# Kernel optimization log

Hardware: AMD Instinct MI355X
Metric: run time of the kernel (lower is better)

Reference implementation:

```python
import jax, jax.numpy as jnp
import numpy as np

B, T, C = 2, 4096, 768
H = 12
D = C // H  # head_dim = 64
SCALE = np.sqrt(D).astype(np.float32)


def setup_inputs() -> dict:
    key = jax.random.key(0)
    ks = jax.random.split(key, 5)
    s = 0.02
    return {
        "x": jax.random.normal(ks[0], (B, T, C), dtype=jnp.float32),
        "Wqkv": jax.random.normal(ks[1], (C, 3 * C), dtype=jnp.float32) * s,
        "bqkv": jnp.zeros((3 * C,), dtype=jnp.float32),
        "Wout": jax.random.normal(ks[2], (C, C), dtype=jnp.float32) * s,
        "bout": jnp.zeros((C,), dtype=jnp.float32),
    }


def reference(x, Wqkv, bqkv, Wout, bout):
    Bx, Tx, Cx = x.shape
    qkv = x @ Wqkv + bqkv                                   # [B,T,3C]
    qkv = qkv.reshape(Bx, Tx, 3, H, D)
    q, k, v = [jnp.moveaxis(qkv[:, :, i], 2, 1) for i in range(3)]  # each [B,H,T,D]
    attn = jnp.einsum("bhqd,bhkd->bhqk", q, k) / SCALE      # [B,H,T,T]
    causal = jnp.tril(jnp.ones((Tx, Tx), dtype=bool))
    attn = jnp.where(causal, attn, jnp.float32(-jnp.inf))
    attn = jax.nn.softmax(attn, axis=-1)
    out = jnp.einsum("bhqk,bhkd->bhqd", attn, v)            # [B,H,T,D]
    out = jnp.moveaxis(out, 1, 2).reshape(Bx, Tx, Cx)       # [B,T,C]
    return out @ Wout + bout
```

## Files before the change

kernel.cpp:

```cpp
#include <hip/hip_runtime.h>
#include <hip/hip_bf16.h>

#define T_DIM 4096
#define H_N 12
#define D_H 64
#define C_DIM 768
#define B_N 2

typedef short bf16x8 __attribute__((ext_vector_type(8)));
typedef float f32x4 __attribute__((ext_vector_type(4)));

__device__ __forceinline__ short f2bf(float f) {
    union { float f; unsigned u; } x; x.f = f;
    unsigned r = x.u + 0x7fffu + ((x.u >> 16) & 1u);
    return (short)(r >> 16);
}
__device__ __forceinline__ unsigned pk2bf(float a, float b) {
    union { float f; unsigned u; } x, y; x.f = a; y.f = b;
    unsigned ua = x.u + 0x7fffu + ((x.u >> 16) & 1u);
    unsigned ub = y.u + 0x7fffu + ((y.u >> 16) & 1u);
    return (ua >> 16) | (ub & 0xffff0000u);
}
__device__ __forceinline__ unsigned pktrunc(float lo, float hi) {
    union { float f; unsigned u; } a, b; a.f = lo; b.f = hi;
    return __builtin_amdgcn_perm(b.u, a.u, 0x07060302u);
}
__device__ __forceinline__ float bf2f(short s) {
    union { unsigned u; float f; } x; x.u = ((unsigned)(unsigned short)s) << 16;
    return x.f;
}

__device__ __forceinline__ void async_copy16(const void* g, void* l) {
    __builtin_amdgcn_global_load_lds(
        (const __attribute__((address_space(1))) unsigned*)g,
        (__attribute__((address_space(3))) unsigned*)l, 16, 0, 0);
}

#define Q_SCALE 0.18033688011112042f

__global__ __launch_bounds__(256) void xconv_kernel(
    const float* __restrict__ x, short* __restrict__ xb)
{
    size_t i = ((size_t)blockIdx.x * 256 + threadIdx.x) * 8;
    float4 a = *(const float4*)(x + i);
    float4 b = *(const float4*)(x + i + 4);
    unsigned pk[4];
    pk[0] = pk2bf(a.x, a.y); pk[1] = pk2bf(a.z, a.w);
    pk[2] = pk2bf(b.x, b.y); pk[3] = pk2bf(b.z, b.w);
    *(uint4*)(xb + i) = *(uint4*)pk;
}

__global__ __launch_bounds__(256) void wtrans_kernel(
    const float* __restrict__ W, short* __restrict__ Wt, int K, int N)
{
    const int wave = threadIdx.x >> 6, lane = threadIdx.x & 63;
    const int n = blockIdx.x * 256 + wave * 64 + lane;
    const int k0 = blockIdx.y * 128;
    for (int k = k0; k < k0 + 128; k += 8) {
        unsigned pk[4];
#pragma unroll
        for (int j = 0; j < 4; ++j)
            pk[j] = pk2bf(W[(size_t)(k + 2 * j) * N + n],
                          W[(size_t)(k + 2 * j + 1) * N + n]);
        *(uint4*)(Wt + (size_t)n * K + k) = *(uint4*)pk;
    }
}

__global__ __launch_bounds__(256) void qkv_kernel(
    const short* __restrict__ xb, const short* __restrict__ Wb,
    const float* __restrict__ bias,
    short* __restrict__ Qo, short* __restrict__ Ko, short* __restrict__ Vto)
{
    __shared__ short As[128 * 32];
    __shared__ short Bs[128 * 32];
    __shared__ short Vs[64][136];

    const int tid  = threadIdx.x;
    const int wave = tid >> 6, lane = tid & 63;
    const int quad = lane >> 4, l16 = lane & 15;
    const int wm = wave >> 1, wn = wave & 1;
    const int m0 = blockIdx.y * 128, n0 = blockIdx.x * 128;
    const int lrow = lane >> 2, lcc = lane & 3;

    f32x4 acc[4][4];
#pragma unroll
    for (int i = 0; i < 4; ++i)
#pragma unroll
        for (int j = 0; j < 4; ++j) acc[i][j] = (f32x4){0.f, 0.f, 0.f, 0.f};

    for (int k0 = 0; k0 < 768; k0 += 32) {
        __syncthreads();
#pragma unroll
        for (int i = 0; i < 2; ++i) {
            const int sbase = wave * 128 + i * 64;
            const int row = wave * 32 + i * 16 + lrow;
            async_copy16(xb + (size_t)(m0 + row) * 768 + k0 + lcc * 8, &As[sbase * 8]);
            async_copy16(Wb + (size_t)(n0 + row) * 768 + k0 + lcc * 8, &Bs[sbase * 8]);
        }
        asm volatile("s_waitcnt vmcnt(0)" ::: "memory");
        __syncthreads();

        bf16x8 af[4], bfr[4];
#pragma unroll
        for (int t = 0; t < 4; ++t)
            af[t] = *(const bf16x8*)&As[(wm * 64 + t * 16 + l16) * 32 + quad * 8];
#pragma unroll
        for (int t = 0; t < 4; ++t)
            bfr[t] = *(const bf16x8*)&Bs[(wn * 64 + t * 16 + l16) * 32 + quad * 8];
#pragma unroll
        for (int mt = 0; mt < 4; ++mt)
#pragma unroll
            for (int nt = 0; nt < 4; ++nt)
                acc[mt][nt] = __builtin_amdgcn_mfma_f32_16x16x32_bf16(
                    af[mt], bfr[nt], acc[mt][nt], 0, 0, 0);
    }

    if (n0 < 1536) {
#pragma unroll
        for (int nt = 0; nt < 4; ++nt) {
            int n = n0 + wn * 64 + nt * 16 + l16;
            float bv = bias[n];
            int which = n >= 768;
            int cw = n - which * 768;
            int h = cw >> 6, d = cw & 63;
            float scale = which ? 1.0f : Q_SCALE;
            short* dst = which ? Ko : Qo;
#pragma unroll
            for (int mt = 0; mt < 4; ++mt) {
#pragma unroll
                for (int reg = 0; reg < 4; ++reg) {
                    int m = m0 + wm * 64 + mt * 16 + quad * 4 + reg;
                    int b = m >> 12, t = m & 4095;
                    dst[(size_t)((b * H_N + h) * T_DIM + t) * D_H + d] =
                        f2bf((acc[mt][nt][reg] + bv) * scale);
                }
            }
        }
    } else {
        const int b = m0 >> 12, t0 = m0 & 4095;
        for (int p = 0; p < 2; ++p) {
            if (wn == p) {
#pragma unroll
                for (int nt = 0; nt < 4; ++nt) {
                    int n = n0 + wn * 64 + nt * 16 + l16;
                    float bv = bias[n];
#pragma unroll
                    for (int mt = 0; mt < 4; ++mt)
#pragma unroll
                        for (int reg = 0; reg < 4; ++reg)
                            Vs[nt * 16 + l16][wm * 64 + mt * 16 + quad * 4 + reg] =
                                f2bf(acc[mt][nt][reg] + bv);
                }
            }
            __syncthreads();
            int hh = ((n0 - 1536) >> 6) + p;
#pragma unroll
            for (int cc = tid; cc < 512; cc += 256) {
                int d = cc >> 3, part = cc & 7;
                bf16x8 v0 = *(const bf16x8*)&Vs[d][part * 16];
                bf16x8 v1 = *(const bf16x8*)&Vs[d][part * 16 + 8];
                size_t dst = ((size_t)(b * H_N + hh) * D_H + d) * T_DIM + t0 + part * 16;
                *(bf16x8*)(Vto + dst) = v0;
                *(bf16x8*)(Vto + dst + 8) = v1;
            }
            __syncthreads();
        }
    }
}

__global__ __launch_bounds__(256) void attn_partial_kernel(
    const short* __restrict__ Q, const short* __restrict__ K,
    const short* __restrict__ Vt, short* __restrict__ Opart,
    float* __restrict__ Lbuf)
{
    __shared__ short KsT[2][4096];
    __shared__ short VsT[2][4096];
    __shared__ short Ps[4][32][76];

    const int tid  = threadIdx.x;
    const int wave = tid >> 6, lane = tid & 63;
    const int quad = lane >> 4, l16 = lane & 15;
    const int bh = blockIdx.y;
    const int rr = blockIdx.x;

    int qj, ci;
    if (rr < 12) { qj = 12 + rr; ci = 0; }
    else if (rr < 28) { int t = rr - 12; qj = 24 + (t >> 1); ci = t & 1; }
    else {
        int t = rr - 28;
        if (t < 8) { int g = t >> 1, b = t & 1; int m = 12 - g;
                     qj = b ? (11 + m) : (m - 1); }
        else { int tt = t - 8; int g = tt / 3, b = tt - 3 * g; int m = 8 - g;
               qj = (b == 0) ? (m - 1) : ((b == 1) ? (11 + m) : (23 + m)); }
        ci = qj / 12;
    }
    const int q0 = qj * 128;
    const int kvStart = ci * 1536;
    const int kvEnd = min(kvStart + 1536, q0 + 128);
    const int ntiles = (kvEnd - kvStart) >> 6;
    const int off = (qj < 12) ? qj : ((qj < 24) ? 12 + (qj - 12) * 2
                                               : 36 + (qj - 24) * 3);
    const int s = bh * 60 + off + ci;
    const size_t base = (size_t)bh * T_DIM * D_H;
    const int row0 = q0 + wave * 32;

    bf16x8 qf[2][2];
#pragma unroll
    for (int qt = 0; qt < 2; ++qt)
#pragma unroll
        for (int ks = 0; ks < 2; ++ks)
            qf[qt][ks] = *(const bf16x8*)(
                Q + base + (size_t)(row0 + qt * 16 + l16) * 64 + ks * 32 + quad * 8);

    bf16x8 ones;
#pragma unroll
    for (int j = 0; j < 8; ++j) ones[j] = (short)0x3F80;

    f32x4 oacc[2][4], lacc[2];
#pragma unroll
    for (int qt = 0; qt < 2; ++qt) {
        lacc[qt] = (f32x4){0.f, 0.f, 0.f, 0.f};
#pragma unroll
        for (int nt = 0; nt < 4; ++nt) oacc[qt][nt] = (f32x4){0.f, 0.f, 0.f, 0.f};
    }

    const int srow = (wave * 128 + lane) >> 3;
    const int scol0 = (lane & 7) ^ (srow & 7);
    const int srow1 = (wave * 128 + 64 + lane) >> 3;
    const int scol1 = (lane & 7) ^ (srow1 & 7);

    {
        const int kv0 = kvStart;
        async_copy16(K + base + (size_t)(kv0 + srow) * 64 + scol0 * 8,
                     &KsT[0][(wave * 128) * 8]);
        async_copy16(Vt + base + (size_t)srow * T_DIM + kv0 + scol0 * 8,
                     &VsT[0][(wave * 128) * 8]);
        async_copy16(K + base + (size_t)(kv0 + srow1) * 64 + scol1 * 8,
                     &KsT[0][(wave * 128 + 64) * 8]);
        async_copy16(Vt + base + (size_t)srow1 * T_DIM + kv0 + scol1 * 8,
                     &VsT[0][(wave * 128 + 64) * 8]);
    }

    int buf = 0;
    for (int it = 0; it < ntiles; ++it) {
        const int kv0 = kvStart + it * 64;

        asm volatile("s_waitcnt vmcnt(0)" ::: "memory");
        asm volatile("s_barrier" ::: "memory");

        if (it + 1 < ntiles) {
            const int kn = kv0 + 64;
            async_copy16(K + base + (size_t)(kn + srow) * 64 + scol0 * 8,
                         &KsT[buf ^ 1][(wave * 128) * 8]);
            async_copy16(Vt + base + (size_t)srow * T_DIM + kn + scol0 * 8,
                         &VsT[buf ^ 1][(wave * 128) * 8]);
            async_copy16(K + base + (size_t)(kn + srow1) * 64 + scol1 * 8,
                         &KsT[buf ^ 1][(wave * 128 + 64) * 8]);
            async_copy16(Vt + base + (size_t)srow1 * T_DIM + kn + scol1 * 8,
                         &VsT[buf ^ 1][(wave * 128 + 64) * 8]);
        }

        if (kv0 <= row0 + 31) {
            const short* Kb = &KsT[buf][0];
            const short* Vb = &VsT[buf][0];

            f32x4 sacc[4][2];
#pragma unroll
            for (int mt = 0; mt < 4; ++mt)
#pragma unroll
                for (int qt = 0; qt < 2; ++qt)
                    sacc[mt][qt] = (f32x4){0.f, 0.f, 0.f, 0.f};
#pragma unroll
            for (int mt = 0; mt < 4; ++mt) {
                int R = mt * 16 + l16;
#pragma unroll
                for (int ks = 0; ks < 2; ++ks) {
                    bf16x8 kf = *(const bf16x8*)&Kb[(R * 8 + ((ks * 4 + quad) ^ (R & 7))) * 8];
                    sacc[mt][0] = __builtin_amdgcn_mfma_f32_16x16x32_bf16(
                        kf, qf[0][ks], sacc[mt][0], 0, 0, 0);
                    sacc[mt][1] = __builtin_amdgcn_mfma_f32_16x16x32_bf16(
                        kf, qf[1][ks], sacc[mt][1], 0, 0, 0);
                }
            }

            if (kv0 + 63 > row0) {
#pragma unroll
                for (int qt = 0; qt < 2; ++qt) {
                    int qrow = row0 + qt * 16 + l16;
#pragma unroll
                    for (int mt = 0; mt < 4; ++mt)
#pragma unroll
                        for (int reg = 0; reg < 4; ++reg)
                            if (kv0 + mt * 16 + quad * 4 + reg > qrow)
                                sacc[mt][qt][reg] = -1e30f;
                }
            }

#pragma unroll
            for (int qt = 0; qt < 2; ++qt) {
#pragma unroll
                for (int mt = 0; mt < 4; ++mt) {
                    float p0 = exp2f(sacc[mt][qt][0]);
                    float p1 = exp2f(sacc[mt][qt][1]);
                    float p2 = exp2f(sacc[mt][qt][2]);
                    float p3 = exp2f(sacc[mt][qt][3]);
                    uint2 pk;
                    pk.x = pktrunc(p0, p1);
                    pk.y = pktrunc(p2, p3);
                    *(uint2*)&Ps[wave][qt * 16 + l16][mt * 16 + quad * 4] = pk;
                }
            }

            asm volatile("s_waitcnt lgkmcnt(0)" ::: "memory");

#pragma unroll
            for (int ks = 0; ks < 2; ++ks) {
                bf16x8 pa0 = *(const bf16x8*)&Ps[wave][l16][ks * 32 + quad * 8];
                bf16x8 pa1 = *(const bf16x8*)&Ps[wave][16 + l16][ks * 32 + quad * 8];
                lacc[0] = __builtin_amdgcn_mfma_f32_16x16x32_bf16(pa0, ones, lacc[0], 0, 0, 0);
                lacc[1] = __builtin_amdgcn_mfma_f32_16x16x32_bf16(pa1, ones, lacc[1], 0, 0, 0);
#pragma unroll
                for (int nt = 0; nt < 4; ++nt) {
                    int R = nt * 16 + l16;
                    bf16x8 vf = *(const bf16x8*)&Vb[(R * 8 + ((ks * 4 + quad) ^ (R & 7))) * 8];
                    oacc[0][nt] = __builtin_amdgcn_mfma_f32_16x16x32_bf16(
                        pa0, vf, oacc[0][nt], 0, 0, 0);
                    oacc[1][nt] = __builtin_amdgcn_mfma_f32_16x16x32_bf16(
                        pa1, vf, oacc[1][nt], 0, 0, 0);
                }
            }
        }
        buf ^= 1;
    }

    short* op = Opart + (size_t)s * 8192;
#pragma unroll
    for (int qt = 0; qt < 2; ++qt)
#pragma unroll
        for (int nt = 0; nt < 4; ++nt)
#pragma unroll
            for (int reg = 0; reg < 4; ++reg) {
                int row = wave * 32 + qt * 16 + quad * 4 + reg;
                op[row * 64 + nt * 16 + l16] = f2bf(oacc[qt][nt][reg]);
            }
    if (l16 == 0) {
#pragma unroll
        for (int qt = 0; qt < 2; ++qt)
#pragma unroll
            for (int reg = 0; reg < 4; ++reg)
                Lbuf[s * 128 + wave * 32 + qt * 16 + quad * 4 + reg] = lacc[qt][reg];
    }
}

__global__ __launch_bounds__(256) void combine_kernel(
    const short* __restrict__ Opart, const float* __restrict__ Lbuf,
    short* __restrict__ O)
{
    const int tid = threadIdx.x;
    const int qi = blockIdx.x, bh = blockIdx.y;
    const int b = bh / H_N, h = bh - b * H_N;
    const int r = tid >> 2, cg = (tid & 3) * 16;
    const int qj = qi >> 1;
    const int riu = (qi & 1) * 64 + r;
    const int off = (qj < 12) ? qj : ((qj < 24) ? 12 + (qj - 12) * 2
                                               : 36 + (qj - 24) * 3);
    const int nc = qj / 12 + 1;
    const int s0 = bh * 60 + off;

    float l = 0.f;
    float res[16];
#pragma unroll
    for (int j = 0; j < 16; ++j) res[j] = 0.f;

    for (int ci = 0; ci < nc; ++ci) {
        const int su = s0 + ci;
        l += Lbuf[su * 128 + riu];
        const short* p = Opart + (size_t)su * 8192 + riu * 64 + cg;
        bf16x8 a0 = *(const bf16x8*)p;
        bf16x8 a1 = *(const bf16x8*)(p + 8);
#pragma unroll
        for (int j = 0; j < 8; ++j) { res[j] += bf2f(a0[j]); res[8 + j] += bf2f(a1[j]); }
    }

    float inv = 1.0f / l;
    unsigned pk[8];
#pragma unroll
    for (int j = 0; j < 8; ++j) pk[j] = pk2bf(res[2 * j] * inv, res[2 * j + 1] * inv);
    size_t o = ((size_t)b * T_DIM + qi * 64 + r) * C_DIM + h * 64 + cg;
    *(uint4*)(O + o)     = *(uint4*)&pk[0];
    *(uint4*)(O + o + 8) = *(uint4*)&pk[4];
}

__global__ __launch_bounds__(256) void out_kernel(
    const short* __restrict__ A, const short* __restrict__ Wb,
    const float* __restrict__ bias, float* __restrict__ out)
{
    __shared__ short As[128 * 32];
    __shared__ short Bs[128 * 32];

    const int tid  = threadIdx.x;
    const int wave = tid >> 6, lane = tid & 63;
    const int quad = lane >> 4, l16 = lane & 15;
    const int wm = wave >> 1, wn = wave & 1;
    const int m0 = blockIdx.y * 128, n0 = blockIdx.x * 128;
    const int lrow = lane >> 2, lcc = lane & 3;

    f32x4 acc[4][4];
#pragma unroll
    for (int i = 0; i < 4; ++i)
#pragma unroll
        for (int j = 0; j < 4; ++j) acc[i][j] = (f32x4){0.f, 0.f, 0.f, 0.f};

    for (int k0 = 0; k0 < 768; k0 += 32) {
        __syncthreads();
#pragma unroll
        for (int i = 0; i < 2; ++i) {
            const int sbase = wave * 128 + i * 64;
            const int row = wave * 32 + i * 16 + lrow;
            async_copy16(A  + (size_t)(m0 + row) * 768 + k0 + lcc * 8, &As[sbase * 8]);
            async_copy16(Wb + (size_t)(n0 + row) * 768 + k0 + lcc * 8, &Bs[sbase * 8]);
        }
        asm volatile("s_waitcnt vmcnt(0)" ::: "memory");
        __syncthreads();

        bf16x8 af[4], bfr[4];
#pragma unroll
        for (int t = 0; t < 4; ++t)
            af[t] = *(const bf16x8*)&As[(wm * 64 + t * 16 + l16) * 32 + quad * 8];
#pragma unroll
        for (int t = 0; t < 4; ++t)
            bfr[t] = *(const bf16x8*)&Bs[(wn * 64 + t * 16 + l16) * 32 + quad * 8];
#pragma unroll
        for (int mt = 0; mt < 4; ++mt)
#pragma unroll
            for (int nt = 0; nt < 4; ++nt)
                acc[mt][nt] = __builtin_amdgcn_mfma_f32_16x16x32_bf16(
                    af[mt], bfr[nt], acc[mt][nt], 0, 0, 0);
    }

#pragma unroll
    for (int nt = 0; nt < 4; ++nt) {
        int n = n0 + wn * 64 + nt * 16 + l16;
        float bv = bias[n];
#pragma unroll
        for (int mt = 0; mt < 4; ++mt) {
#pragma unroll
            for (int reg = 0; reg < 4; ++reg) {
                int m = m0 + wm * 64 + mt * 16 + quad * 4 + reg;
                out[(size_t)m * 768 + n] = acc[mt][nt][reg] + bv;
            }
        }
    }
}

extern "C" void kernel_launch(void* const* d_in, const int* in_sizes, int n_in,
                              void* d_out, int out_size, void* d_ws, size_t ws_size,
                              hipStream_t stream) {
    const float* x    = (const float*)d_in[0];
    const float* Wqkv = (const float*)d_in[1];
    const float* bqkv = (const float*)d_in[2];
    const float* Wout = (const float*)d_in[3];
    const float* bout = (const float*)d_in[4];
    float* out = (float*)d_out;

    const size_t per = (size_t)B_N * H_N * T_DIM * D_H;
    short* Q      = (short*)d_ws;
    short* K      = Q + per;
    short* Vt     = K + per;
    short* Woutb  = Vt + per;
    short* xb     = Woutb + (size_t)768 * 768;
    short* Wqkvb  = xb + per;
    short* Opart  = xb;
    float* Lbuf   = (float*)(Opart + (size_t)1440 * 8192);
    short* O      = Q;

    xconv_kernel<<<dim3(3072), 256, 0, stream>>>(x, xb);
    wtrans_kernel<<<dim3(9, 6), 256, 0, stream>>>(Wqkv, Wqkvb, 768, 2304);
    wtrans_kernel<<<dim3(3, 6), 256, 0, stream>>>(Wout, Woutb, 768, 768);
    qkv_kernel<<<dim3(18, 64), 256, 0, stream>>>(xb, Wqkvb, bqkv, Q, K, Vt);
    attn_partial_kernel<<<dim3(60, 24), 256, 0, stream>>>(Q, K, Vt, Opart, Lbuf);
    combine_kernel<<<dim3(64, 24), 256, 0, stream>>>(Opart, Lbuf, O);
    out_kernel<<<dim3(6, 64), 256, 0, stream>>>(O, Woutb, bout, out);
}
```

Measured before the change: 336.3 us.

## Double-buffer GEMM LDS tiles and merge prep conversions into one launch

The QKV and output-projection GEMMs now double-buffer their LDS tiles. Each iteration issues the async global-to-LDS copy for the next K-slice before computing on the current one, so one barrier per step replaces two and load latency is meant to overlap with MFMA work. The x conversion and the two weight transpose/convert kernels are merged into a single prep launch to cut launch overhead. LDS use per block grows to 32 KB, and correctness depends on the single barrier ordering the reads of the previous buffer before it is overwritten.

```diff
diff --git a/kernel.cpp b/kernel.cpp
--- a/kernel.cpp
+++ b/kernel.cpp
@@ -38,31 +38,35 @@
 
 #define Q_SCALE 0.18033688011112042f
 
-__global__ __launch_bounds__(256) void xconv_kernel(
-    const float* __restrict__ x, short* __restrict__ xb)
+__global__ __launch_bounds__(256) void prep_kernel(
+    const float* __restrict__ x, short* __restrict__ xb,
+    const float* __restrict__ Wqkv, short* __restrict__ Wqkvb,
+    const float* __restrict__ Wout, short* __restrict__ Woutb)
 {
-    size_t i = ((size_t)blockIdx.x * 256 + threadIdx.x) * 8;
-    float4 a = *(const float4*)(x + i);
-    float4 b = *(const float4*)(x + i + 4);
-    unsigned pk[4];
-    pk[0] = pk2bf(a.x, a.y); pk[1] = pk2bf(a.z, a.w);
-    pk[2] = pk2bf(b.x, b.y); pk[3] = pk2bf(b.z, b.w);
-    *(uint4*)(xb + i) = *(uint4*)pk;
-}
-
-__global__ __launch_bounds__(256) void wtrans_kernel(
-    const float* __restrict__ W, short* __restrict__ Wt, int K, int N)
-{
+    const int bid = blockIdx.x;
+    if (bid < 3072) {
+        size_t i = ((size_t)bid * 256 + threadIdx.x) * 8;
+        float4 a = *(const float4*)(x + i);
+        float4 b = *(const float4*)(x + i + 4);
+        unsigned pk[4];
+        pk[0] = pk2bf(a.x, a.y); pk[1] = pk2bf(a.z, a.w);
+        pk[2] = pk2bf(b.x, b.y); pk[3] = pk2bf(b.z, b.w);
+        *(uint4*)(xb + i) = *(uint4*)pk;
+        return;
+    }
+    const float* W; short* Wt; int N, bx, by;
+    if (bid < 3126) { W = Wqkv; Wt = Wqkvb; N = 2304; bx = (bid - 3072) % 9; by = (bid - 3072) / 9; }
+    else            { W = Wout; Wt = Woutb; N = 768;  bx = (bid - 3126) % 3; by = (bid - 3126) / 3; }
     const int wave = threadIdx.x >> 6, lane = threadIdx.x & 63;
-    const int n = blockIdx.x * 256 + wave * 64 + lane;
-    const int k0 = blockIdx.y * 128;
+    const int n = bx * 256 + wave * 64 + lane;
+    const int k0 = by * 128;
     for (int k = k0; k < k0 + 128; k += 8) {
         unsigned pk[4];
 #pragma unroll
         for (int j = 0; j < 4; ++j)
             pk[j] = pk2bf(W[(size_t)(k + 2 * j) * N + n],
                           W[(size_t)(k + 2 * j + 1) * N + n]);
-        *(uint4*)(Wt + (size_t)n * K + k) = *(uint4*)pk;
+        *(uint4*)(Wt + (size_t)n * 768 + k) = *(uint4*)pk;
     }
 }
 
@@ -71,9 +75,7 @@
     const float* __restrict__ bias,
     short* __restrict__ Qo, short* __restrict__ Ko, short* __restrict__ Vto)
 {
-    __shared__ short As[128 * 32];
-    __shared__ short Bs[128 * 32];
-    __shared__ short Vs[64][136];
+    __shared__ __align__(16) short S[16384];
 
     const int tid  = threadIdx.x;
     const int wave = tid >> 6, lane = tid & 63;
@@ -88,31 +90,41 @@
 #pragma unroll
         for (int j = 0; j < 4; ++j) acc[i][j] = (f32x4){0.f, 0.f, 0.f, 0.f};
 
-    for (int k0 = 0; k0 < 768; k0 += 32) {
-        __syncthreads();
+    auto issue = [&](int k0, int buf) {
 #pragma unroll
         for (int i = 0; i < 2; ++i) {
             const int sbase = wave * 128 + i * 64;
             const int row = wave * 32 + i * 16 + lrow;
-            async_copy16(xb + (size_t)(m0 + row) * 768 + k0 + lcc * 8, &As[sbase * 8]);
-            async_copy16(Wb + (size_t)(n0 + row) * 768 + k0 + lcc * 8, &Bs[sbase * 8]);
-        }
+            async_copy16(xb + (size_t)(m0 + row) * 768 + k0 + lcc * 8,
+                         &S[buf * 4096 + sbase * 8]);
+            async_copy16(Wb + (size_t)(n0 + row) * 768 + k0 + lcc * 8,
+                         &S[8192 + buf * 4096 + sbase * 8]);
+        }
+    };
+
+    issue(0, 0);
+    int buf = 0;
+    for (int k0 = 0; k0 < 768; k0 += 32) {
         asm volatile("s_waitcnt vmcnt(0)" ::: "memory");
-        __syncthreads();
-
+        asm volatile("s_barrier" ::: "memory");
+        if (k0 + 32 < 768) issue(k0 + 32, buf ^ 1);
+
+        const short* Ab = &S[buf * 4096];
+        const short* Bb = &S[8192 + buf * 4096];
         bf16x8 af[4], bfr[4];
 #pragma unroll
         for (int t = 0; t < 4; ++t)
-            af[t] = *(const bf16x8*)&As[(wm * 64 + t * 16 + l16) * 32 + quad * 8];
+            af[t] = *(const bf16x8*)&Ab[(wm * 64 + t * 16 + l16) * 32 + quad * 8];
 #pragma unroll
         for (int t = 0; t < 4; ++t)
-            bfr[t] = *(const bf16x8*)&Bs[(wn * 64 + t * 16 + l16) * 32 + quad * 8];
+            bfr[t] = *(const bf16x8*)&Bb[(wn * 64 + t * 16 + l16) * 32 + quad * 8];
 #pragma unroll
         for (int mt = 0; mt < 4; ++mt)
 #pragma unroll
             for (int nt = 0; nt < 4; ++nt)
                 acc[mt][nt] = __builtin_amdgcn_mfma_f32_16x16x32_bf16(
                     af[mt], bfr[nt], acc[mt][nt], 0, 0, 0);
+        buf ^= 1;
     }
 
     if (n0 < 1536) {
@@ -137,6 +149,8 @@
             }
         }
     } else {
+        __syncthreads();
+        short (*Vs)[136] = (short (*)[136])S;
         const int b = m0 >> 12, t0 = m0 & 4095;
         for (int p = 0; p < 2; ++p) {
             if (wn == p) {
@@ -395,8 +409,7 @@
     const short* __restrict__ A, const short* __restrict__ Wb,
     const float* __restrict__ bias, float* __restrict__ out)
 {
-    __shared__ short As[128 * 32];
-    __shared__ short Bs[128 * 32];
+    __shared__ __align__(16) short S[16384];
 
     const int tid  = threadIdx.x;
     const int wave = tid >> 6, lane = tid & 63;
@@ -411,31 +424,41 @@
 #pragma unroll
         for (int j = 0; j < 4; ++j) acc[i][j] = (f32x4){0.f, 0.f, 0.f, 0.f};
 
-    for (int k0 = 0; k0 < 768; k0 += 32) {
-        __syncthreads();
+    auto issue = [&](int k0, int buf) {
 #pragma unroll
         for (int i = 0; i < 2; ++i) {
             const int sbase = wave * 128 + i * 64;
             const int row = wave * 32 + i * 16 + lrow;
-            async_copy16(A  + (size_t)(m0 + row) * 768 + k0 + lcc * 8, &As[sbase * 8]);
-            async_copy16(Wb + (size_t)(n0 + row) * 768 + k0 + lcc * 8, &Bs[sbase * 8]);
-        }
+            async_copy16(A  + (size_t)(m0 + row) * 768 + k0 + lcc * 8,
+                         &S[buf * 4096 + sbase * 8]);
+            async_copy16(Wb + (size_t)(n0 + row) * 768 + k0 + lcc * 8,
+                         &S[8192 + buf * 4096 + sbase * 8]);
+        }
+    };
+
+    issue(0, 0);
+    int buf = 0;
+    for (int k0 = 0; k0 < 768; k0 += 32) {
         asm volatile("s_waitcnt vmcnt(0)" ::: "memory");
-        __syncthreads();
-
+        asm volatile("s_barrier" ::: "memory");
+        if (k0 + 32 < 768) issue(k0 + 32, buf ^ 1);
+
+        const short* Ab = &S[buf * 4096];
+        const short* Bb = &S[8192 + buf * 4096];
         bf16x8 af[4], bfr[4];
 #pragma unroll
         for (int t = 0; t < 4; ++t)
-            af[t] = *(const bf16x8*)&As[(wm * 64 + t * 16 + l16) * 32 + quad * 8];
+            af[t] = *(const bf16x8*)&Ab[(wm * 64 + t * 16 + l16) * 32 + quad * 8];
 #pragma unroll
         for (int t = 0; t < 4; ++t)
-            bfr[t] = *(const bf16x8*)&Bs[(wn * 64 + t * 16 + l16) * 32 + quad * 8];
+            bfr[t] = *(const bf16x8*)&Bb[(wn * 64 + t * 16 + l16) * 32 + quad * 8];
 #pragma unroll
         for (int mt = 0; mt < 4; ++mt)
 #pragma unroll
             for (int nt = 0; nt < 4; ++nt)
                 acc[mt][nt] = __builtin_amdgcn_mfma_f32_16x16x32_bf16(
                     af[mt], bfr[nt], acc[mt][nt], 0, 0, 0);
+        buf ^= 1;
     }
 
 #pragma unroll
@@ -474,9 +497,7 @@
     float* Lbuf   = (float*)(Opart + (size_t)1440 * 8192);
     short* O      = Q;
 
-    xconv_kernel<<<dim3(3072), 256, 0, stream>>>(x, xb);
-    wtrans_kernel<<<dim3(9, 6), 256, 0, stream>>>(Wqkv, Wqkvb, 768, 2304);
-    wtrans_kernel<<<dim3(3, 6), 256, 0, stream>>>(Wout, Woutb, 768, 768);
+    prep_kernel<<<dim3(3144), 256, 0, stream>>>(x, xb, Wqkv, Wqkvb, Wout, Woutb);
     qkv_kernel<<<dim3(18, 64), 256, 0, stream>>>(xb, Wqkvb, bqkv, Q, K, Vt);
     attn_partial_kernel<<<dim3(60, 24), 256, 0, stream>>>(Q, K, Vt, Opart, Lbuf);
     combine_kernel<<<dim3(64, 24), 256, 0, stream>>>(Opart, Lbuf, O);
```

After: 347.9 us. 1.03x slower.
